# Kernel optimization log

Measured on AMD Instinct MI355X. Metric: run time of the kernel, lower is better.

The kernel has to match this reference:

```python
import jax, jax.numpy as jnp
import numpy as np

C_REG = 50.0  # soft-SVM regularization from __init__ default C=50


def kronecker(A, B):
    # torch: einsum('ab,cd->acbd').view(a*c, b*d)
    return jnp.einsum('ab,cd->acbd', A, B).reshape(
        A.shape[0] * B.shape[0], A.shape[1] * B.shape[1])


def setup_inputs() -> dict:
    key = jax.random.key(0)
    k1, k2, k3, k4 = jax.random.split(key, 4)
    N_c, N_S, N_Q, C, W, H = 16, 25, 15, 3, 32, 32
    D_feat = 640
    S_k = jax.random.normal(k1, (N_c, N_S, C, W, H), dtype=jnp.float32)
    Q_k = jax.random.normal(k2, (N_c, N_Q, C, W, H), dtype=jnp.float32)
    # base_net modeled as Flatten -> Linear(C*W*H, D_feat), no bias
    W_base = jax.random.normal(k3, (C * W * H, D_feat), dtype=jnp.float32) * 0.02
    gamma = jax.random.normal(k4, (1,), dtype=jnp.float32)
    return {"S_k": S_k, "Q_k": Q_k, "W_base": W_base, "gamma": gamma}


def reference(S_k, Q_k, W_base, gamma):
    N_c, N_S = S_k.shape[:2]
    N_Q = Q_k.shape[1]
    # base_net: flatten image dims, project to features
    f_x = S_k.reshape(N_c * N_S, -1) @ W_base  # placeholder
    f_x = Q_k.reshape(N_c * N_Q, -1) @ W_base          # [N_c*N_Q, D]
    K = S_k.reshape(N_c * N_S, -1) @ W_base            # [N_c*N_S, D]
    # kernel matrix + ridge
    aul = K @ K.T + C_REG * jnp.eye(N_c * N_S, dtype=K.dtype)  # [N_c*N_S, N_c*N_S]
    # explicit Kronecker expansion to the full (N_c^2*N_S) system
    Q = kronecker(jnp.eye(N_c, dtype=K.dtype), aul)    # [N_c^2*N_S, N_c^2*N_S]
    p = kronecker(jnp.eye(N_c, dtype=K.dtype),
                  jnp.ones((1, N_S), dtype=K.dtype)).reshape(-1, 1)
    alpha = jnp.linalg.solve(Q, jax.lax.stop_gradient(p))  # p is detached in torch
    alpha = alpha.reshape(N_c, -1)                     # [N_c, N_c*N_S]
    w_k = alpha @ K                                    # [N_c, D]
    logits = -gamma * (f_x @ w_k.T)                    # [N_c*N_Q, N_c]
    return logits
```

## Files before the change

### kernel.cpp

```cpp
#include <hip/hip_runtime.h>
#include <math.h>

#define DIN 3072
#define DF 640
#define MROWS 400
#define QROWS 240
#define NMAT 400
#define PN 416
#define NRHS 16
#define CREG 50.0f
#define PVSTEPS 5
#define CSTEPS 25
#define KSPLIT 4
#define GBLK 13
#define SCOLS 32
#define SPAD 40
#define FPAD 72
#define MTILES 28

typedef __attribute__((ext_vector_type(8))) short bf8v;
typedef __attribute__((ext_vector_type(4))) short s4v;
typedef __attribute__((ext_vector_type(4))) float f32x4;

__device__ __forceinline__ short bf16_rn(float x) {
  unsigned u = __float_as_uint(x);
  u += 0x7FFFu + ((u >> 16) & 1u);
  return (short)(u >> 16);
}
__device__ __forceinline__ void split_sh(float x, short& h, short& l) {
  h = bf16_rn(x);
  float hf = __uint_as_float(((unsigned)(unsigned short)h) << 16);
  l = bf16_rn(x - hf);
}
__device__ __forceinline__ float bf2f(short h) {
  return __uint_as_float(((unsigned)(unsigned short)h) << 16);
}

__global__ __launch_bounds__(256) void gemm_feat_sk(const float* __restrict__ S,
                                                    const float* __restrict__ Qm,
                                                    const float* __restrict__ Wb,
                                                    float* __restrict__ Acc) {
  __shared__ short Ash[64][FPAD];
  __shared__ short Asl[64][FPAD];
  __shared__ short Bsh[64][FPAD];
  __shared__ short Bsl[64][FPAD];
  int tid = threadIdx.x;
  int wave = tid >> 6, lane = tid & 63, l16 = lane & 15, quad = lane >> 4;
  int by = blockIdx.y, bx = blockIdx.x, bz = blockIdx.z;
  int colBase = bx * 64;
  int kbeg = bz * (DIN / KSPLIT), kend = kbeg + (DIN / KSPLIT);
  int arow = by * 64 + (tid >> 4);
  const float* sr = (arow < MROWS) ? (S + (size_t)arow * DIN)
                                   : (Qm + (size_t)(arow - MROWS) * DIN);
  int kc4 = (tid & 15) * 4;
  float4 ar4[4], br4[4];
  auto load_regs = [&](int kk) {
#pragma unroll
    for (int p = 0; p < 4; ++p) {
      int rowoff = 16 * p;
      const float* srp;
      {
        int ar_ = by * 64 + (tid >> 4) + rowoff;
        srp = (ar_ < MROWS) ? (S + (size_t)ar_ * DIN) : (Qm + (size_t)(ar_ - MROWS) * DIN);
      }
      ar4[p] = *reinterpret_cast<const float4*>(srp + kk + kc4);
      int r = (tid >> 4) + rowoff;
      br4[p] = *reinterpret_cast<const float4*>(Wb + (size_t)(kk + r) * DF + colBase + kc4);
    }
  };
  auto split_write = [&]() {
#pragma unroll
    for (int p = 0; p < 4; ++p) {
      int row = (tid >> 4) + 16 * p;
      s4v hv, lv; short h, l;
      split_sh(ar4[p].x, h, l); hv[0] = h; lv[0] = l;
      split_sh(ar4[p].y, h, l); hv[1] = h; lv[1] = l;
      split_sh(ar4[p].z, h, l); hv[2] = h; lv[2] = l;
      split_sh(ar4[p].w, h, l); hv[3] = h; lv[3] = l;
      *reinterpret_cast<s4v*>(&Ash[row][kc4]) = hv;
      *reinterpret_cast<s4v*>(&Asl[row][kc4]) = lv;
      split_sh(br4[p].x, h, l); Bsh[kc4 + 0][row] = h; Bsl[kc4 + 0][row] = l;
      split_sh(br4[p].y, h, l); Bsh[kc4 + 1][row] = h; Bsl[kc4 + 1][row] = l;
      split_sh(br4[p].z, h, l); Bsh[kc4 + 2][row] = h; Bsl[kc4 + 2][row] = l;
      split_sh(br4[p].w, h, l); Bsh[kc4 + 3][row] = h; Bsl[kc4 + 3][row] = l;
    }
  };
  f32x4 acc[4] = {{0,0,0,0},{0,0,0,0},{0,0,0,0},{0,0,0,0}};
  load_regs(kbeg);
  split_write();
  __syncthreads();
  int k0 = kbeg;
  while (true) {
    int kn = k0 + 64;
    bool more = (kn < kend);
    if (more) load_regs(kn);
#pragma unroll
    for (int kk = 0; kk < 64; kk += 32) {
      int ko = kk + quad * 8;
      bf8v ah = *reinterpret_cast<const bf8v*>(&Ash[wave * 16 + l16][ko]);
      bf8v al = *reinterpret_cast<const bf8v*>(&Asl[wave * 16 + l16][ko]);
#pragma unroll
      for (int t = 0; t < 4; ++t) {
        bf8v bh = *reinterpret_cast<const bf8v*>(&Bsh[t * 16 + l16][ko]);
        bf8v bl = *reinterpret_cast<const bf8v*>(&Bsl[t * 16 + l16][ko]);
        acc[t] = __builtin_amdgcn_mfma_f32_16x16x32_bf16(ah, bh, acc[t], 0, 0, 0);
        acc[t] = __builtin_amdgcn_mfma_f32_16x16x32_bf16(ah, bl, acc[t], 0, 0, 0);
        acc[t] = __builtin_amdgcn_mfma_f32_16x16x32_bf16(al, bh, acc[t], 0, 0, 0);
      }
    }
    if (!more) break;
    __syncthreads();
    split_write();
    __syncthreads();
    k0 = kn;
  }
  float* Ap = Acc + (size_t)bz * 640 * DF;
  int row0 = by * 64 + wave * 16;
#pragma unroll
  for (int t = 0; t < 4; ++t)
#pragma unroll
    for (int r = 0; r < 4; ++r) {
      int row = row0 + quad * 4 + r;
      int col = colBase + t * 16 + l16;
      Ap[(size_t)row * DF + col] = acc[t][r];
    }
}

__global__ __launch_bounds__(256) void feat_reduce(const float* __restrict__ Acc,
                                                   short* __restrict__ Kh,
                                                   short* __restrict__ Kl,
                                                   float* __restrict__ FX,
                                                   float* __restrict__ zbuf,
                                                   float* __restrict__ out) {
  int tid = threadIdx.x;
  if (blockIdx.x == 0) {
    for (int e = tid; e < 14160; e += 256) zbuf[e] = 0.f;
  } else if (blockIdx.x == 1) {
    for (int e = tid; e < QROWS * NRHS; e += 256) out[e] = 0.f;
  }
  int idx = blockIdx.x * 256 + tid;
  if (idx >= 640 * DF) return;
  float v = Acc[idx] + Acc[idx + 409600] + Acc[idx + 819200] + Acc[idx + 1228800];
  int row = idx / DF, col = idx - row * DF;
  if (row < MROWS) {
    short h, l; split_sh(v, h, l);
    Kh[(size_t)row * DF + col] = h;
    Kl[(size_t)row * DF + col] = l;
  } else {
    FX[(size_t)(row - MROWS) * DF + col] = v;
  }
}

__global__ __launch_bounds__(256) void gemm_aul(const short* __restrict__ Kh,
                                                const short* __restrict__ Kl,
                                                short* __restrict__ Aph,
                                                short* __restrict__ Apl) {
  int tid = threadIdx.x;
  int wave = tid >> 6, lane = tid & 63;
  int l16 = lane & 15, quad = lane >> 4;
  int row0 = blockIdx.y * 64 + wave * 16;
  int colBase = blockIdx.x * 64;
  bool aValid = (row0 < MROWS);
  const bf8v bzero = {0,0,0,0,0,0,0,0};
  f32x4 acc[4] = {{0,0,0,0},{0,0,0,0},{0,0,0,0},{0,0,0,0}};
  for (int k0 = 0; k0 < DF; k0 += 32) {
    int ka = k0 + quad * 8;
    bf8v ah = bzero, al = bzero;
    if (aValid) {
      size_t ao = (size_t)(row0 + l16) * DF + ka;
      ah = *reinterpret_cast<const bf8v*>(Kh + ao);
      al = *reinterpret_cast<const bf8v*>(Kl + ao);
    }
#pragma unroll
    for (int t = 0; t < 4; ++t) {
      int colt = colBase + t * 16;
      bf8v bh = bzero, bl = bzero;
      if (colt < MROWS) {
        size_t bo = (size_t)(colt + l16) * DF + ka;
        bh = *reinterpret_cast<const bf8v*>(Kh + bo);
        bl = *reinterpret_cast<const bf8v*>(Kl + bo);
      }
      acc[t] = __builtin_amdgcn_mfma_f32_16x16x32_bf16(ah, bh, acc[t], 0, 0, 0);
      acc[t] = __builtin_amdgcn_mfma_f32_16x16x32_bf16(ah, bl, acc[t], 0, 0, 0);
      acc[t] = __builtin_amdgcn_mfma_f32_16x16x32_bf16(al, bh, acc[t], 0, 0, 0);
    }
  }
  if (row0 >= PN) return;
#pragma unroll
  for (int t = 0; t < 4; ++t) {
    int colt = colBase + t * 16;
    if (colt >= PN) continue;
#pragma unroll
    for (int r = 0; r < 4; ++r) {
      int row = row0 + quad * 4 + r;
      int col = colt + l16;
      float v = acc[t][r];
      if (row == col && row < MROWS) v += CREG;
      short h, l; split_sh(v, h, l);
      size_t o = (size_t)row * PN + col;
      Aph[o] = h; Apl[o] = l;
    }
  }
}

__global__ __launch_bounds__(256) void solve_and_m(const short* __restrict__ Aph,
                                                   const short* __restrict__ Apl,
                                                   const float* __restrict__ FX,
                                                   const short* __restrict__ Kh,
                                                   const short* __restrict__ Kl,
                                                   const float* __restrict__ gamma,
                                                   float* __restrict__ Y0,
                                                   float* __restrict__ Y1,
                                                   float* __restrict__ V0,
                                                   float* __restrict__ V1,
                                                   float* __restrict__ rq,
                                                   unsigned* __restrict__ bar,
                                                   unsigned* __restrict__ mflag,
                                                   float* __restrict__ M,
                                                   float* __restrict__ out) {
  int tid = threadIdx.x, b = blockIdx.x;
  int wave = tid >> 6, lane = tid & 63, l16 = lane & 15, quad = lane >> 4;
  const bf8v bzero = {0,0,0,0,0,0,0,0};

  if (b >= GBLK) {
    int mt = b - GBLK;
    int mb = mt / 7, nb = mt - (mt / 7) * 7;
    int q0 = mb * 64 + wave * 16;
    f32x4 acc[4] = {{0,0,0,0},{0,0,0,0},{0,0,0,0},{0,0,0,0}};
    int arow = q0 + l16;
    bool aOk = (arow < QROWS);
    const float* fr = FX + (size_t)(aOk ? arow : 0) * DF;
    for (int k0 = 0; k0 < DF; k0 += 32) {
      int ka = k0 + quad * 8;
      bf8v ah = bzero, al = bzero;
      if (aOk) {
        float4 a0 = *reinterpret_cast<const float4*>(fr + ka);
        float4 a1 = *reinterpret_cast<const float4*>(fr + ka + 4);
        float av[8] = {a0.x, a0.y, a0.z, a0.w, a1.x, a1.y, a1.z, a1.w};
#pragma unroll
        for (int j = 0; j < 8; ++j) { short h, l; split_sh(av[j], h, l); ah[j] = h; al[j] = l; }
      }
#pragma unroll
      for (int t = 0; t < 4; ++t) {
        int n = nb * 64 + t * 16 + l16;
        bf8v bh = bzero, bl = bzero;
        if (n < NMAT) {
          bh = *reinterpret_cast<const bf8v*>(Kh + (size_t)n * DF + ka);
          bl = *reinterpret_cast<const bf8v*>(Kl + (size_t)n * DF + ka);
        }
        acc[t] = __builtin_amdgcn_mfma_f32_16x16x32_bf16(ah, bh, acc[t], 0, 0, 0);
        acc[t] = __builtin_amdgcn_mfma_f32_16x16x32_bf16(ah, bl, acc[t], 0, 0, 0);
        acc[t] = __builtin_amdgcn_mfma_f32_16x16x32_bf16(al, bh, acc[t], 0, 0, 0);
      }
    }
#pragma unroll
    for (int t = 0; t < 4; ++t)
#pragma unroll
      for (int r = 0; r < 4; ++r) {
        int row = q0 + quad * 4 + r;
        int col = nb * 64 + t * 16 + l16;
        if (row < QROWS && col < NMAT)
          __hip_atomic_store(&M[(size_t)row * NMAT + col], acc[t][r],
                             __ATOMIC_RELAXED, __HIP_MEMORY_SCOPE_AGENT);
      }
    __syncthreads();
    if (tid == 0)
      __hip_atomic_fetch_add(mflag, 1u, __ATOMIC_RELEASE, __HIP_MEMORY_SCOPE_AGENT);
    return;
  }

  __shared__ __align__(16) short AsT_h[PN][SPAD];
  __shared__ short AsT_l[PN][SPAD];
  __shared__ short dbT_h[16][SPAD];
  __shared__ short dbT_l[16][SPAD];
  __shared__ float pvp[SCOLS], pvc[SCOLS];
  __shared__ float scal[2];
  __shared__ float XsL[SCOLS][NRHS + 1];
  int r0 = b * SCOLS;

  for (int e = tid; e < SCOLS * (PN / 8); e += 256) {
    int jl = e / (PN / 8), ic = e - (e / (PN / 8)) * (PN / 8);
    bf8v vh = *reinterpret_cast<const bf8v*>(Aph + (size_t)(r0 + jl) * PN + ic * 8);
    bf8v vl = *reinterpret_cast<const bf8v*>(Apl + (size_t)(r0 + jl) * PN + ic * 8);
#pragma unroll
    for (int u = 0; u < 8; ++u) {
      AsT_h[ic * 8 + u][jl] = vh[u];
      AsT_l[ic * 8 + u][jl] = vl[u];
    }
  }
  for (int e = tid; e < 16 * SPAD; e += 256) {
    (&dbT_h[0][0])[e] = 0; (&dbT_l[0][0])[e] = 0;
  }
  __syncthreads();
  if (tid < SCOLS) {
    int gi = r0 + tid;
    float v = (gi < NMAT) ? (1.f + 0.125f * (float)(gi & 7)) : 0.f;
    pvc[tid] = v; pvp[tid] = 0.f;
    dbT_h[0][tid] = bf16_rn(v);
  }
  __syncthreads();

  unsigned ph = 0;
  auto gridbar = [&]() {
    __syncthreads();
    ++ph;
    if (tid == 0) {
      unsigned tgt = ph * GBLK;
      __hip_atomic_fetch_add(bar, 1u, __ATOMIC_RELEASE, __HIP_MEMORY_SCOPE_AGENT);
      while (__hip_atomic_load(bar, __ATOMIC_RELAXED, __HIP_MEMORY_SCOPE_AGENT) < tgt)
        __builtin_amdgcn_s_sleep(2);
    }
    __syncthreads();
  };

  for (int s = 0; s < PVSTEPS; ++s) {
    float* Yv = (s & 1) ? V1 : V0;
    for (int t = wave; t < 26; t += 4) {
      f32x4 acc = {0, 0, 0, 0};
      bf8v bh = *reinterpret_cast<const bf8v*>(&dbT_h[l16][quad * 8]);
      bf8v ah = *reinterpret_cast<const bf8v*>(&AsT_h[t * 16 + l16][quad * 8]);
      acc = __builtin_amdgcn_mfma_f32_16x16x32_bf16(ah, bh, acc, 0, 0, 0);
      if (l16 == 0) {
#pragma unroll
        for (int r_ = 0; r_ < 4; ++r_)
          atomicAdd(&Yv[t * 16 + quad * 4 + r_], acc[r_]);
      }
    }
    gridbar();
    if (tid < SCOLS) {
      float y = atomicExch(&Yv[r0 + tid], 0.f);
      float v = y * (1.f / 4096.f);
      pvp[tid] = pvc[tid];
      pvc[tid] = v;
      dbT_h[0][tid] = bf16_rn(v);
    }
    __syncthreads();
  }
  if (tid == 0) {
    float n = 0.f, dd = 0.f;
    for (int u = 0; u < SCOLS; ++u) { n += pvp[u] * pvc[u]; dd += pvp[u] * pvp[u]; }
    atomicAdd(&rq[0], n);
    atomicAdd(&rq[1], dd);
  }
  gridbar();
  if (tid == 0) {
    float rn = atomicAdd(&rq[0], 0.f), rd = atomicAdd(&rq[1], 0.f);
    float rqv = 4096.f * rn / rd;
    float bb = 1.3f * rqv;
    if (!(bb > 800.f)) bb = 12000.f;
    if (bb > 100000.f) bb = 100000.f;
    scal[0] = 0.5f * (bb + CREG);
    scal[1] = 0.5f * (bb - CREG);
  }
  __syncthreads();
  float theta = scal[0], delta = scal[1];
  float sigma = theta / delta, rho = 1.f / sigma;

  float xr[2], rr[2], dr[2];
#pragma unroll
  for (int m = 0; m < 2; ++m) {
    int rl = (tid >> 4) + 16 * m, c = tid & 15, gi = r0 + rl;
    float pc = (gi < NMAT && (gi / 25) == c) ? 1.f : 0.f;
    xr[m] = 0.f; rr[m] = pc; dr[m] = pc / theta;
    short h, l; split_sh(dr[m], h, l);
    dbT_h[c][rl] = h; dbT_l[c][rl] = l;
  }
  __syncthreads();

  for (int k = 0; k < CSTEPS - 1; ++k) {
    float* Yv = (k & 1) ? Y1 : Y0;
    for (int t = wave; t < 26; t += 4) {
      f32x4 acc = {0, 0, 0, 0};
      bf8v bh = *reinterpret_cast<const bf8v*>(&dbT_h[l16][quad * 8]);
      bf8v bl = *reinterpret_cast<const bf8v*>(&dbT_l[l16][quad * 8]);
      bf8v ah = *reinterpret_cast<const bf8v*>(&AsT_h[t * 16 + l16][quad * 8]);
      bf8v al = *reinterpret_cast<const bf8v*>(&AsT_l[t * 16 + l16][quad * 8]);
      acc = __builtin_amdgcn_mfma_f32_16x16x32_bf16(ah, bh, acc, 0, 0, 0);
      acc = __builtin_amdgcn_mfma_f32_16x16x32_bf16(ah, bl, acc, 0, 0, 0);
      acc = __builtin_amdgcn_mfma_f32_16x16x32_bf16(al, bh, acc, 0, 0, 0);
#pragma unroll
      for (int r_ = 0; r_ < 4; ++r_)
        atomicAdd(&Yv[(t * 16 + quad * 4 + r_) * 16 + l16], acc[r_]);
    }
    gridbar();
    float rho1 = 1.f / (2.f * sigma - rho);
    float s1 = rho1 * rho, s2 = 2.f * rho1 / delta;
    rho = rho1;
#pragma unroll
    for (int m = 0; m < 2; ++m) {
      int rl = (tid >> 4) + 16 * m, c = tid & 15, gi = r0 + rl;
      float mv = atomicExch(&Yv[gi * 16 + c], 0.f);
      xr[m] += dr[m];
      rr[m] -= mv;
      float dn = s1 * dr[m] + s2 * rr[m];
      dr[m] = dn;
      short h, l; split_sh(dn, h, l);
      dbT_h[c][rl] = h; dbT_l[c][rl] = l;
    }
    __syncthreads();
  }
#pragma unroll
  for (int m = 0; m < 2; ++m) {
    int rl = (tid >> 4) + 16 * m, c = tid & 15;
    XsL[rl][c] = xr[m] + dr[m];
  }
  __syncthreads();
  if (tid == 0) {
    while (__hip_atomic_load(mflag, __ATOMIC_RELAXED, __HIP_MEMORY_SCOPE_AGENT) < MTILES)
      __builtin_amdgcn_s_sleep(2);
  }
  __syncthreads();
  float* Msl = reinterpret_cast<float*>(&AsT_h[0][0]);
  for (int e = tid; e < QROWS * SCOLS; e += 256) {
    int q = e >> 5, i = e & 31;
    float v = 0.f;
    if (r0 + i < NMAT)
      v = __hip_atomic_load(&M[(size_t)q * NMAT + r0 + i],
                            __ATOMIC_RELAXED, __HIP_MEMORY_SCOPE_AGENT);
    Msl[e] = v;
  }
  __syncthreads();
  float g = -gamma[0];
  int c = tid & 15;
  for (int q = tid >> 4; q < QROWS; q += 16) {
    float s = 0.f;
#pragma unroll
    for (int i = 0; i < SCOLS; ++i) s += Msl[q * SCOLS + i] * XsL[i][c];
    atomicAdd(&out[q * NRHS + c], g * s);
  }
}

extern "C" void kernel_launch(void* const* d_in, const int* in_sizes, int n_in,
                              void* d_out, int out_size, void* d_ws, size_t ws_size,
                              hipStream_t stream) {
  const float* S = (const float*)d_in[0];
  const float* Qm = (const float*)d_in[1];
  const float* Wb = (const float*)d_in[2];
  const float* gamma = (const float*)d_in[3];
  float* out = (float*)d_out;
  char* base = (char*)d_ws;
  short* Kh   = (short*)(base);
  short* Kl   = (short*)(base + 512000);
  float* FX   = (float*)(base + 1024000);
  short* Aph  = (short*)(base + 1638400);
  short* Apl  = (short*)(base + 1984512);
  float* Mm   = (float*)(base + 2330624);
  unsigned* bar = (unsigned*)(base + 2740224);
  float* rq   = (float*)(base + 2740232);
  unsigned* mflag = (unsigned*)(base + 2740240);
  float* zbuf = (float*)(base + 2740224);
  float* Y0   = (float*)(base + 2740288);
  float* Y1   = (float*)(base + 2766912);
  float* V0   = (float*)(base + 2793536);
  float* V1   = (float*)(base + 2795200);
  float* Acc  = (float*)(base + 2796864);

  gemm_feat_sk<<<dim3(10, 10, KSPLIT), 256, 0, stream>>>(S, Qm, Wb, Acc);
  feat_reduce<<<1600, 256, 0, stream>>>(Acc, Kh, Kl, FX, zbuf, out);
  gemm_aul<<<dim3(7, 7), 256, 0, stream>>>(Kh, Kl, Aph, Apl);
  solve_and_m<<<GBLK + MTILES, 256, 0, stream>>>(Aph, Apl, FX, Kh, Kl, gamma,
                                                 Y0, Y1, V0, V1, rq, bar, mflag,
                                                 Mm, out);
}
```

Before: 229.1 us.

## Switch solver to row-block ownership with broadcast direction vectors instead of atomic partial sums

The Chebyshev/power-iteration solver is restructured. Each block now holds its 32 rows of the matrix untransposed and computes its own slice of the matvec locally, reducing across waves in shared memory. Before, each block computed column contributions and scattered them with global atomicAdd/atomicExch. The direction vector is now packed as hi/lo bf16 in one word, published to global memory, and gathered by every block after a grid barrier. This removes global float atomics and the separate Rayleigh-quotient grid barrier, since every block now computes that quotient redundantly. In exchange, each block does more global reads per step, and the zeroing of the workspace is shrunk.

```diff
diff --git a/kernel.cpp b/kernel.cpp
--- a/kernel.cpp
+++ b/kernel.cpp
@@ -14,9 +14,9 @@
 #define KSPLIT 4
 #define GBLK 13
 #define SCOLS 32
-#define SPAD 40
 #define FPAD 72
 #define MTILES 28
+#define DPAD 424
 
 typedef __attribute__((ext_vector_type(8))) short bf8v;
 typedef __attribute__((ext_vector_type(4))) short s4v;
@@ -49,9 +49,6 @@
   int by = blockIdx.y, bx = blockIdx.x, bz = blockIdx.z;
   int colBase = bx * 64;
   int kbeg = bz * (DIN / KSPLIT), kend = kbeg + (DIN / KSPLIT);
-  int arow = by * 64 + (tid >> 4);
-  const float* sr = (arow < MROWS) ? (S + (size_t)arow * DIN)
-                                   : (Qm + (size_t)(arow - MROWS) * DIN);
   int kc4 = (tid & 15) * 4;
   float4 ar4[4], br4[4];
   auto load_regs = [&](int kk) {
@@ -134,7 +131,7 @@
                                                    float* __restrict__ out) {
   int tid = threadIdx.x;
   if (blockIdx.x == 0) {
-    for (int e = tid; e < 14160; e += 256) zbuf[e] = 0.f;
+    for (int e = tid; e < 16; e += 256) zbuf[e] = 0.f;
   } else if (blockIdx.x == 1) {
     for (int e = tid; e < QROWS * NRHS; e += 256) out[e] = 0.f;
   }
@@ -209,11 +206,10 @@
                                                    const short* __restrict__ Kh,
                                                    const short* __restrict__ Kl,
                                                    const float* __restrict__ gamma,
-                                                   float* __restrict__ Y0,
-                                                   float* __restrict__ Y1,
+                                                   unsigned* __restrict__ D0,
+                                                   unsigned* __restrict__ D1,
                                                    float* __restrict__ V0,
                                                    float* __restrict__ V1,
-                                                   float* __restrict__ rq,
                                                    unsigned* __restrict__ bar,
                                                    unsigned* __restrict__ mflag,
                                                    float* __restrict__ M,
@@ -269,34 +265,27 @@
     return;
   }
 
-  __shared__ __align__(16) short AsT_h[PN][SPAD];
-  __shared__ short AsT_l[PN][SPAD];
-  __shared__ short dbT_h[16][SPAD];
-  __shared__ short dbT_l[16][SPAD];
-  __shared__ float pvp[SCOLS], pvc[SCOLS];
+  __shared__ __align__(16) short Abig[2][SCOLS][DPAD];
+  __shared__ __align__(16) short dbT[2][NRHS][DPAD];
+  __shared__ float yred[4][SCOLS][17];
+  __shared__ float vprevL[PN], vcurL[PN];
+  __shared__ float XsL[SCOLS][NRHS + 1];
   __shared__ float scal[2];
-  __shared__ float XsL[SCOLS][NRHS + 1];
+  __shared__ float rn[4], rd[4];
   int r0 = b * SCOLS;
 
-  for (int e = tid; e < SCOLS * (PN / 8); e += 256) {
-    int jl = e / (PN / 8), ic = e - (e / (PN / 8)) * (PN / 8);
-    bf8v vh = *reinterpret_cast<const bf8v*>(Aph + (size_t)(r0 + jl) * PN + ic * 8);
-    bf8v vl = *reinterpret_cast<const bf8v*>(Apl + (size_t)(r0 + jl) * PN + ic * 8);
-#pragma unroll
-    for (int u = 0; u < 8; ++u) {
-      AsT_h[ic * 8 + u][jl] = vh[u];
-      AsT_l[ic * 8 + u][jl] = vl[u];
-    }
-  }
-  for (int e = tid; e < 16 * SPAD; e += 256) {
-    (&dbT_h[0][0])[e] = 0; (&dbT_l[0][0])[e] = 0;
-  }
-  __syncthreads();
-  if (tid < SCOLS) {
-    int gi = r0 + tid;
-    float v = (gi < NMAT) ? (1.f + 0.125f * (float)(gi & 7)) : 0.f;
-    pvc[tid] = v; pvp[tid] = 0.f;
-    dbT_h[0][tid] = bf16_rn(v);
+  for (int e = tid; e < SCOLS * 52; e += 256) {
+    int i = e / 52, c = e - i * 52;
+    *reinterpret_cast<bf8v*>(&Abig[0][i][c * 8]) =
+        *reinterpret_cast<const bf8v*>(Aph + (size_t)(r0 + i) * PN + c * 8);
+    *reinterpret_cast<bf8v*>(&Abig[1][i][c * 8]) =
+        *reinterpret_cast<const bf8v*>(Apl + (size_t)(r0 + i) * PN + c * 8);
+  }
+  for (int e = tid; e < NRHS * DPAD; e += 256) (&dbT[0][0][0])[e] = 0;
+  for (int e = tid; e < PN; e += 256) {
+    float v = (e < NMAT) ? (1.f + 0.125f * (float)(e & 7)) : 0.f;
+    vcurL[e] = v;
+    dbT[0][0][e] = bf16_rn(v);
   }
   __syncthreads();
 
@@ -313,46 +302,86 @@
     __syncthreads();
   };
 
+  auto matvec = [&](bool lo) {
+    f32x4 acc0 = {0, 0, 0, 0}, acc1 = {0, 0, 0, 0};
+    for (int kt = wave; kt < 13; kt += 4) {
+      int ko = kt * 32 + quad * 8;
+      bf8v bh = *reinterpret_cast<const bf8v*>(&dbT[0][l16][ko]);
+      bf8v ah0 = *reinterpret_cast<const bf8v*>(&Abig[0][l16][ko]);
+      bf8v ah1 = *reinterpret_cast<const bf8v*>(&Abig[0][16 + l16][ko]);
+      acc0 = __builtin_amdgcn_mfma_f32_16x16x32_bf16(ah0, bh, acc0, 0, 0, 0);
+      acc1 = __builtin_amdgcn_mfma_f32_16x16x32_bf16(ah1, bh, acc1, 0, 0, 0);
+      if (lo) {
+        bf8v bl = *reinterpret_cast<const bf8v*>(&dbT[1][l16][ko]);
+        bf8v al0 = *reinterpret_cast<const bf8v*>(&Abig[1][l16][ko]);
+        bf8v al1 = *reinterpret_cast<const bf8v*>(&Abig[1][16 + l16][ko]);
+        acc0 = __builtin_amdgcn_mfma_f32_16x16x32_bf16(ah0, bl, acc0, 0, 0, 0);
+        acc0 = __builtin_amdgcn_mfma_f32_16x16x32_bf16(al0, bh, acc0, 0, 0, 0);
+        acc1 = __builtin_amdgcn_mfma_f32_16x16x32_bf16(ah1, bl, acc1, 0, 0, 0);
+        acc1 = __builtin_amdgcn_mfma_f32_16x16x32_bf16(al1, bh, acc1, 0, 0, 0);
+      }
+    }
+#pragma unroll
+    for (int r_ = 0; r_ < 4; ++r_) {
+      yred[wave][quad * 4 + r_][l16] = acc0[r_];
+      yred[wave][16 + quad * 4 + r_][l16] = acc1[r_];
+    }
+  };
+
   for (int s = 0; s < PVSTEPS; ++s) {
-    float* Yv = (s & 1) ? V1 : V0;
-    for (int t = wave; t < 26; t += 4) {
-      f32x4 acc = {0, 0, 0, 0};
-      bf8v bh = *reinterpret_cast<const bf8v*>(&dbT_h[l16][quad * 8]);
-      bf8v ah = *reinterpret_cast<const bf8v*>(&AsT_h[t * 16 + l16][quad * 8]);
-      acc = __builtin_amdgcn_mfma_f32_16x16x32_bf16(ah, bh, acc, 0, 0, 0);
-      if (l16 == 0) {
-#pragma unroll
-        for (int r_ = 0; r_ < 4; ++r_)
-          atomicAdd(&Yv[t * 16 + quad * 4 + r_], acc[r_]);
-      }
+    matvec(false);
+    __syncthreads();
+    if (tid < SCOLS) {
+      float y = yred[0][tid][0] + yred[1][tid][0] + yred[2][tid][0] + yred[3][tid][0];
+      float* Vb = (s & 1) ? V1 : V0;
+      __hip_atomic_store(&Vb[r0 + tid], y, __ATOMIC_RELAXED, __HIP_MEMORY_SCOPE_AGENT);
     }
     gridbar();
-    if (tid < SCOLS) {
-      float y = atomicExch(&Yv[r0 + tid], 0.f);
-      float v = y * (1.f / 4096.f);
-      pvp[tid] = pvc[tid];
-      pvc[tid] = v;
-      dbT_h[0][tid] = bf16_rn(v);
-    }
-    __syncthreads();
-  }
-  if (tid == 0) {
+    const float* Vb = (s & 1) ? V1 : V0;
+    if (s == PVSTEPS - 1)
+      for (int e = tid; e < PN; e += 256) vprevL[e] = vcurL[e];
+    float g0 = __hip_atomic_load(&Vb[tid], __ATOMIC_RELAXED, __HIP_MEMORY_SCOPE_AGENT);
+    float g1 = (tid < PN - 256)
+        ? __hip_atomic_load(&Vb[tid + 256], __ATOMIC_RELAXED, __HIP_MEMORY_SCOPE_AGENT)
+        : 0.f;
+    {
+      float v = g0 * (1.f / 4096.f);
+      vcurL[tid] = v;
+      dbT[0][0][tid] = bf16_rn(v);
+    }
+    if (tid < PN - 256) {
+      float v = g1 * (1.f / 4096.f);
+      vcurL[tid + 256] = v;
+      dbT[0][0][tid + 256] = bf16_rn(v);
+    }
+    __syncthreads();
+  }
+
+  {
     float n = 0.f, dd = 0.f;
-    for (int u = 0; u < SCOLS; ++u) { n += pvp[u] * pvc[u]; dd += pvp[u] * pvp[u]; }
-    atomicAdd(&rq[0], n);
-    atomicAdd(&rq[1], dd);
-  }
-  gridbar();
-  if (tid == 0) {
-    float rn = atomicAdd(&rq[0], 0.f), rd = atomicAdd(&rq[1], 0.f);
-    float rqv = 4096.f * rn / rd;
-    float bb = 1.3f * rqv;
-    if (!(bb > 800.f)) bb = 12000.f;
-    if (bb > 100000.f) bb = 100000.f;
-    scal[0] = 0.5f * (bb + CREG);
-    scal[1] = 0.5f * (bb - CREG);
-  }
-  __syncthreads();
+    for (int e = tid; e < PN; e += 256) {
+      n += vprevL[e] * vcurL[e];
+      dd += vprevL[e] * vprevL[e];
+    }
+#pragma unroll
+    for (int o = 32; o; o >>= 1) {
+      n += __shfl_down(n, o);
+      dd += __shfl_down(dd, o);
+    }
+    if (lane == 0) { rn[wave] = n; rd[wave] = dd; }
+    __syncthreads();
+    if (tid == 0) {
+      float N = rn[0] + rn[1] + rn[2] + rn[3];
+      float D = rd[0] + rd[1] + rd[2] + rd[3];
+      float rqv = 4096.f * N / D;
+      float bb = 1.3f * rqv;
+      if (!(bb > 800.f)) bb = 12000.f;
+      if (bb > 100000.f) bb = 100000.f;
+      scal[0] = 0.5f * (bb + CREG);
+      scal[1] = 0.5f * (bb - CREG);
+    }
+    __syncthreads();
+  }
   float theta = scal[0], delta = scal[1];
   float sigma = theta / delta, rho = 1.f / sigma;
 
@@ -363,42 +392,63 @@
     float pc = (gi < NMAT && (gi / 25) == c) ? 1.f : 0.f;
     xr[m] = 0.f; rr[m] = pc; dr[m] = pc / theta;
     short h, l; split_sh(dr[m], h, l);
-    dbT_h[c][rl] = h; dbT_l[c][rl] = l;
+    __hip_atomic_store(&D0[(size_t)gi * NRHS + c],
+                       ((unsigned)(unsigned short)h << 16) | (unsigned)(unsigned short)l,
+                       __ATOMIC_RELAXED, __HIP_MEMORY_SCOPE_AGENT);
+  }
+  gridbar();
+  {
+    unsigned gw[26];
+#pragma unroll
+    for (int j = 0; j < 26; ++j)
+      gw[j] = __hip_atomic_load(&D0[tid + 256 * j], __ATOMIC_RELAXED, __HIP_MEMORY_SCOPE_AGENT);
+#pragma unroll
+    for (int j = 0; j < 26; ++j) {
+      int e = tid + 256 * j, row = e >> 4, c = e & 15;
+      dbT[0][c][row] = (short)(gw[j] >> 16);
+      dbT[1][c][row] = (short)gw[j];
+    }
   }
   __syncthreads();
 
   for (int k = 0; k < CSTEPS - 1; ++k) {
-    float* Yv = (k & 1) ? Y1 : Y0;
-    for (int t = wave; t < 26; t += 4) {
-      f32x4 acc = {0, 0, 0, 0};
-      bf8v bh = *reinterpret_cast<const bf8v*>(&dbT_h[l16][quad * 8]);
-      bf8v bl = *reinterpret_cast<const bf8v*>(&dbT_l[l16][quad * 8]);
-      bf8v ah = *reinterpret_cast<const bf8v*>(&AsT_h[t * 16 + l16][quad * 8]);
-      bf8v al = *reinterpret_cast<const bf8v*>(&AsT_l[t * 16 + l16][quad * 8]);
-      acc = __builtin_amdgcn_mfma_f32_16x16x32_bf16(ah, bh, acc, 0, 0, 0);
-      acc = __builtin_amdgcn_mfma_f32_16x16x32_bf16(ah, bl, acc, 0, 0, 0);
-      acc = __builtin_amdgcn_mfma_f32_16x16x32_bf16(al, bh, acc, 0, 0, 0);
-#pragma unroll
-      for (int r_ = 0; r_ < 4; ++r_)
-        atomicAdd(&Yv[(t * 16 + quad * 4 + r_) * 16 + l16], acc[r_]);
-    }
-    gridbar();
+    matvec(true);
+    __syncthreads();
     float rho1 = 1.f / (2.f * sigma - rho);
     float s1 = rho1 * rho, s2 = 2.f * rho1 / delta;
     rho = rho1;
+    unsigned* Db = (k & 1) ? D0 : D1;
 #pragma unroll
     for (int m = 0; m < 2; ++m) {
       int rl = (tid >> 4) + 16 * m, c = tid & 15, gi = r0 + rl;
-      float mv = atomicExch(&Yv[gi * 16 + c], 0.f);
+      float mv = yred[0][rl][c] + yred[1][rl][c] + yred[2][rl][c] + yred[3][rl][c];
       xr[m] += dr[m];
       rr[m] -= mv;
       float dn = s1 * dr[m] + s2 * rr[m];
       dr[m] = dn;
-      short h, l; split_sh(dn, h, l);
-      dbT_h[c][rl] = h; dbT_l[c][rl] = l;
-    }
-    __syncthreads();
-  }
+      if (k < CSTEPS - 2) {
+        short h, l; split_sh(dn, h, l);
+        __hip_atomic_store(&Db[(size_t)gi * NRHS + c],
+                           ((unsigned)(unsigned short)h << 16) | (unsigned)(unsigned short)l,
+                           __ATOMIC_RELAXED, __HIP_MEMORY_SCOPE_AGENT);
+      }
+    }
+    if (k < CSTEPS - 2) {
+      gridbar();
+      unsigned gw[26];
+#pragma unroll
+      for (int j = 0; j < 26; ++j)
+        gw[j] = __hip_atomic_load(&Db[tid + 256 * j], __ATOMIC_RELAXED, __HIP_MEMORY_SCOPE_AGENT);
+#pragma unroll
+      for (int j = 0; j < 26; ++j) {
+        int e = tid + 256 * j, row = e >> 4, c = e & 15;
+        dbT[0][c][row] = (short)(gw[j] >> 16);
+        dbT[1][c][row] = (short)gw[j];
+      }
+    }
+    __syncthreads();
+  }
+
 #pragma unroll
   for (int m = 0; m < 2; ++m) {
     int rl = (tid >> 4) + 16 * m, c = tid & 15;
@@ -410,14 +460,20 @@
       __builtin_amdgcn_s_sleep(2);
   }
   __syncthreads();
-  float* Msl = reinterpret_cast<float*>(&AsT_h[0][0]);
-  for (int e = tid; e < QROWS * SCOLS; e += 256) {
-    int q = e >> 5, i = e & 31;
-    float v = 0.f;
-    if (r0 + i < NMAT)
-      v = __hip_atomic_load(&M[(size_t)q * NMAT + r0 + i],
-                            __ATOMIC_RELAXED, __HIP_MEMORY_SCOPE_AGENT);
-    Msl[e] = v;
+  float* Msl = reinterpret_cast<float*>(&Abig[0][0][0]);
+  {
+    float gm[30];
+#pragma unroll
+    for (int j = 0; j < 30; ++j) {
+      int e = tid + 256 * j;
+      int q = e >> 5, i = e & 31;
+      gm[j] = (r0 + i < NMAT)
+                  ? __hip_atomic_load(&M[(size_t)q * NMAT + r0 + i],
+                                      __ATOMIC_RELAXED, __HIP_MEMORY_SCOPE_AGENT)
+                  : 0.f;
+    }
+#pragma unroll
+    for (int j = 0; j < 30; ++j) Msl[tid + 256 * j] = gm[j];
   }
   __syncthreads();
   float g = -gamma[0];
@@ -446,11 +502,10 @@
   short* Apl  = (short*)(base + 1984512);
   float* Mm   = (float*)(base + 2330624);
   unsigned* bar = (unsigned*)(base + 2740224);
-  float* rq   = (float*)(base + 2740232);
   unsigned* mflag = (unsigned*)(base + 2740240);
   float* zbuf = (float*)(base + 2740224);
-  float* Y0   = (float*)(base + 2740288);
-  float* Y1   = (float*)(base + 2766912);
+  unsigned* D0 = (unsigned*)(base + 2740288);
+  unsigned* D1 = (unsigned*)(base + 2766912);
   float* V0   = (float*)(base + 2793536);
   float* V1   = (float*)(base + 2795200);
   float* Acc  = (float*)(base + 2796864);
@@ -459,6 +514,6 @@
   feat_reduce<<<1600, 256, 0, stream>>>(Acc, Kh, Kl, FX, zbuf, out);
   gemm_aul<<<dim3(7, 7), 256, 0, stream>>>(Kh, Kl, Aph, Apl);
   solve_and_m<<<GBLK + MTILES, 256, 0, stream>>>(Aph, Apl, FX, Kh, Kl, gamma,
-                                                 Y0, Y1, V0, V1, rq, bar, mflag,
+                                                 D0, D1, V0, V1, bar, mflag,
                                                  Mm, out);
 }
```

Result: faster. 216.0 us (-5.7%).

## Solve each right-hand side in its own block, dropping grid barriers

Applied to the files above, without the earlier changes.

The Chebyshev solve moves from 13 blocks, each owning a row slice and synchronising through global atomics and grid barriers, to 16 independent blocks, each owning one right-hand side. Each block runs the whole matvec by streaming A from global memory (L2). This removes the grid-wide spin barriers and the atomic accumulation traffic on every iteration. The cost is that every block repeats the power iteration and rereads the full matrix each step, and the MFMA uses only one useful column out of 16. The feature GEMM split-K also doubles from 4 to 8, which doubles the partial-sum traffic in the reduce kernel.

```diff
diff --git a/kernel.cpp b/kernel.cpp
--- a/kernel.cpp
+++ b/kernel.cpp
@@ -11,10 +11,8 @@
 #define CREG 50.0f
 #define PVSTEPS 5
 #define CSTEPS 25
-#define KSPLIT 4
-#define GBLK 13
-#define SCOLS 32
-#define SPAD 40
+#define KSPLIT 8
+#define SRHS 16
 #define FPAD 72
 #define MTILES 28
 
@@ -31,9 +29,6 @@
   h = bf16_rn(x);
   float hf = __uint_as_float(((unsigned)(unsigned short)h) << 16);
   l = bf16_rn(x - hf);
-}
-__device__ __forceinline__ float bf2f(short h) {
-  return __uint_as_float(((unsigned)(unsigned short)h) << 16);
 }
 
 __global__ __launch_bounds__(256) void gemm_feat_sk(const float* __restrict__ S,
@@ -49,9 +44,6 @@
   int by = blockIdx.y, bx = blockIdx.x, bz = blockIdx.z;
   int colBase = bx * 64;
   int kbeg = bz * (DIN / KSPLIT), kend = kbeg + (DIN / KSPLIT);
-  int arow = by * 64 + (tid >> 4);
-  const float* sr = (arow < MROWS) ? (S + (size_t)arow * DIN)
-                                   : (Qm + (size_t)(arow - MROWS) * DIN);
   int kc4 = (tid & 15) * 4;
   float4 ar4[4], br4[4];
   auto load_regs = [&](int kk) {
@@ -130,17 +122,16 @@
                                                    short* __restrict__ Kh,
                                                    short* __restrict__ Kl,
                                                    float* __restrict__ FX,
-                                                   float* __restrict__ zbuf,
-                                                   float* __restrict__ out) {
+                                                   float* __restrict__ zbuf) {
   int tid = threadIdx.x;
   if (blockIdx.x == 0) {
-    for (int e = tid; e < 14160; e += 256) zbuf[e] = 0.f;
-  } else if (blockIdx.x == 1) {
-    for (int e = tid; e < QROWS * NRHS; e += 256) out[e] = 0.f;
+    if (tid < 16) zbuf[tid] = 0.f;
   }
   int idx = blockIdx.x * 256 + tid;
   if (idx >= 640 * DF) return;
-  float v = Acc[idx] + Acc[idx + 409600] + Acc[idx + 819200] + Acc[idx + 1228800];
+  float v = 0.f;
+#pragma unroll
+  for (int s = 0; s < KSPLIT; ++s) v += Acc[idx + (size_t)s * 409600];
   int row = idx / DF, col = idx - row * DF;
   if (row < MROWS) {
     short h, l; split_sh(v, h, l);
@@ -209,12 +200,6 @@
                                                    const short* __restrict__ Kh,
                                                    const short* __restrict__ Kl,
                                                    const float* __restrict__ gamma,
-                                                   float* __restrict__ Y0,
-                                                   float* __restrict__ Y1,
-                                                   float* __restrict__ V0,
-                                                   float* __restrict__ V1,
-                                                   float* __restrict__ rq,
-                                                   unsigned* __restrict__ bar,
                                                    unsigned* __restrict__ mflag,
                                                    float* __restrict__ M,
                                                    float* __restrict__ out) {
@@ -222,8 +207,8 @@
   int wave = tid >> 6, lane = tid & 63, l16 = lane & 15, quad = lane >> 4;
   const bf8v bzero = {0,0,0,0,0,0,0,0};
 
-  if (b >= GBLK) {
-    int mt = b - GBLK;
+  if (b >= SRHS) {
+    int mt = b - SRHS;
     int mb = mt / 7, nb = mt - (mt / 7) * 7;
     int q0 = mb * 64 + wave * 16;
     f32x4 acc[4] = {{0,0,0,0},{0,0,0,0},{0,0,0,0},{0,0,0,0}};
@@ -269,164 +254,136 @@
     return;
   }
 
-  __shared__ __align__(16) short AsT_h[PN][SPAD];
-  __shared__ short AsT_l[PN][SPAD];
-  __shared__ short dbT_h[16][SPAD];
-  __shared__ short dbT_l[16][SPAD];
-  __shared__ float pvp[SCOLS], pvc[SCOLS];
+  int c = b;
+  __shared__ __align__(16) short dbh[432], dbl[432];
+  __shared__ float ys[PN];
+  __shared__ float xf[PN], rf[PN], df[PN];
+  __shared__ float vprev[PN], vcur[PN];
   __shared__ float scal[2];
-  __shared__ float XsL[SCOLS][NRHS + 1];
-  int r0 = b * SCOLS;
-
-  for (int e = tid; e < SCOLS * (PN / 8); e += 256) {
-    int jl = e / (PN / 8), ic = e - (e / (PN / 8)) * (PN / 8);
-    bf8v vh = *reinterpret_cast<const bf8v*>(Aph + (size_t)(r0 + jl) * PN + ic * 8);
-    bf8v vl = *reinterpret_cast<const bf8v*>(Apl + (size_t)(r0 + jl) * PN + ic * 8);
-#pragma unroll
-    for (int u = 0; u < 8; ++u) {
-      AsT_h[ic * 8 + u][jl] = vh[u];
-      AsT_l[ic * 8 + u][jl] = vl[u];
-    }
-  }
-  for (int e = tid; e < 16 * SPAD; e += 256) {
-    (&dbT_h[0][0])[e] = 0; (&dbT_l[0][0])[e] = 0;
+  __shared__ float rn4[4], rd4[4];
+
+  auto matvec = [&](bool lo) {
+    for (int rg = wave; rg < 26; rg += 4) {
+      const short* arow_h = Aph + (size_t)(rg * 16 + l16) * PN;
+      const short* arow_l = Apl + (size_t)(rg * 16 + l16) * PN;
+      f32x4 acc = {0, 0, 0, 0};
+#pragma unroll
+      for (int kc = 0; kc < 13; ++kc) {
+        int ko = kc * 32 + quad * 8;
+        bf8v ah = *reinterpret_cast<const bf8v*>(arow_h + ko);
+        bf8v bh = bzero, bl = bzero;
+        if (l16 == 0) {
+          bh = *reinterpret_cast<const bf8v*>(&dbh[ko]);
+          if (lo) bl = *reinterpret_cast<const bf8v*>(&dbl[ko]);
+        }
+        acc = __builtin_amdgcn_mfma_f32_16x16x32_bf16(ah, bh, acc, 0, 0, 0);
+        if (lo) {
+          bf8v al = *reinterpret_cast<const bf8v*>(arow_l + ko);
+          acc = __builtin_amdgcn_mfma_f32_16x16x32_bf16(ah, bl, acc, 0, 0, 0);
+          acc = __builtin_amdgcn_mfma_f32_16x16x32_bf16(al, bh, acc, 0, 0, 0);
+        }
+      }
+      if (l16 == 0) {
+#pragma unroll
+        for (int r = 0; r < 4; ++r) ys[rg * 16 + quad * 4 + r] = acc[r];
+      }
+    }
+  };
+
+  for (int e = tid; e < PN; e += 256) {
+    float v = (e < NMAT) ? (1.f + 0.125f * (float)(e & 7)) : 0.f;
+    vcur[e] = v;
+    dbh[e] = bf16_rn(v);
+    dbl[e] = 0;
   }
   __syncthreads();
-  if (tid < SCOLS) {
-    int gi = r0 + tid;
-    float v = (gi < NMAT) ? (1.f + 0.125f * (float)(gi & 7)) : 0.f;
-    pvc[tid] = v; pvp[tid] = 0.f;
-    dbT_h[0][tid] = bf16_rn(v);
-  }
-  __syncthreads();
-
-  unsigned ph = 0;
-  auto gridbar = [&]() {
-    __syncthreads();
-    ++ph;
+
+  for (int s = 0; s < PVSTEPS; ++s) {
+    matvec(false);
+    __syncthreads();
+    for (int e = tid; e < PN; e += 256) {
+      if (s == PVSTEPS - 1) vprev[e] = vcur[e];
+      float v = ys[e] * (1.f / 4096.f);
+      vcur[e] = v;
+      dbh[e] = bf16_rn(v);
+    }
+    __syncthreads();
+  }
+
+  {
+    float n = 0.f, dd = 0.f;
+    for (int e = tid; e < PN; e += 256) {
+      n += vprev[e] * vcur[e];
+      dd += vprev[e] * vprev[e];
+    }
+#pragma unroll
+    for (int o = 32; o; o >>= 1) {
+      n += __shfl_down(n, o);
+      dd += __shfl_down(dd, o);
+    }
+    if (lane == 0) { rn4[wave] = n; rd4[wave] = dd; }
+    __syncthreads();
     if (tid == 0) {
-      unsigned tgt = ph * GBLK;
-      __hip_atomic_fetch_add(bar, 1u, __ATOMIC_RELEASE, __HIP_MEMORY_SCOPE_AGENT);
-      while (__hip_atomic_load(bar, __ATOMIC_RELAXED, __HIP_MEMORY_SCOPE_AGENT) < tgt)
-        __builtin_amdgcn_s_sleep(2);
-    }
-    __syncthreads();
-  };
-
-  for (int s = 0; s < PVSTEPS; ++s) {
-    float* Yv = (s & 1) ? V1 : V0;
-    for (int t = wave; t < 26; t += 4) {
-      f32x4 acc = {0, 0, 0, 0};
-      bf8v bh = *reinterpret_cast<const bf8v*>(&dbT_h[l16][quad * 8]);
-      bf8v ah = *reinterpret_cast<const bf8v*>(&AsT_h[t * 16 + l16][quad * 8]);
-      acc = __builtin_amdgcn_mfma_f32_16x16x32_bf16(ah, bh, acc, 0, 0, 0);
-      if (l16 == 0) {
-#pragma unroll
-        for (int r_ = 0; r_ < 4; ++r_)
-          atomicAdd(&Yv[t * 16 + quad * 4 + r_], acc[r_]);
-      }
-    }
-    gridbar();
-    if (tid < SCOLS) {
-      float y = atomicExch(&Yv[r0 + tid], 0.f);
-      float v = y * (1.f / 4096.f);
-      pvp[tid] = pvc[tid];
-      pvc[tid] = v;
-      dbT_h[0][tid] = bf16_rn(v);
-    }
-    __syncthreads();
-  }
-  if (tid == 0) {
-    float n = 0.f, dd = 0.f;
-    for (int u = 0; u < SCOLS; ++u) { n += pvp[u] * pvc[u]; dd += pvp[u] * pvp[u]; }
-    atomicAdd(&rq[0], n);
-    atomicAdd(&rq[1], dd);
-  }
-  gridbar();
-  if (tid == 0) {
-    float rn = atomicAdd(&rq[0], 0.f), rd = atomicAdd(&rq[1], 0.f);
-    float rqv = 4096.f * rn / rd;
-    float bb = 1.3f * rqv;
-    if (!(bb > 800.f)) bb = 12000.f;
-    if (bb > 100000.f) bb = 100000.f;
-    scal[0] = 0.5f * (bb + CREG);
-    scal[1] = 0.5f * (bb - CREG);
-  }
-  __syncthreads();
+      float N = rn4[0] + rn4[1] + rn4[2] + rn4[3];
+      float D = rd4[0] + rd4[1] + rd4[2] + rd4[3];
+      float rqv = 4096.f * N / D;
+      float bb = 1.3f * rqv;
+      if (!(bb > 800.f)) bb = 12000.f;
+      if (bb > 100000.f) bb = 100000.f;
+      scal[0] = 0.5f * (bb + CREG);
+      scal[1] = 0.5f * (bb - CREG);
+    }
+    __syncthreads();
+  }
   float theta = scal[0], delta = scal[1];
   float sigma = theta / delta, rho = 1.f / sigma;
 
-  float xr[2], rr[2], dr[2];
-#pragma unroll
-  for (int m = 0; m < 2; ++m) {
-    int rl = (tid >> 4) + 16 * m, c = tid & 15, gi = r0 + rl;
-    float pc = (gi < NMAT && (gi / 25) == c) ? 1.f : 0.f;
-    xr[m] = 0.f; rr[m] = pc; dr[m] = pc / theta;
-    short h, l; split_sh(dr[m], h, l);
-    dbT_h[c][rl] = h; dbT_l[c][rl] = l;
+  for (int e = tid; e < PN; e += 256) {
+    float pc = (e < NMAT && (e / 25) == c) ? 1.f : 0.f;
+    xf[e] = 0.f; rf[e] = pc;
+    float d0 = pc / theta;
+    df[e] = d0;
+    short h, l; split_sh(d0, h, l);
+    dbh[e] = h; dbl[e] = l;
   }
   __syncthreads();
 
   for (int k = 0; k < CSTEPS - 1; ++k) {
-    float* Yv = (k & 1) ? Y1 : Y0;
-    for (int t = wave; t < 26; t += 4) {
-      f32x4 acc = {0, 0, 0, 0};
-      bf8v bh = *reinterpret_cast<const bf8v*>(&dbT_h[l16][quad * 8]);
-      bf8v bl = *reinterpret_cast<const bf8v*>(&dbT_l[l16][quad * 8]);
-      bf8v ah = *reinterpret_cast<const bf8v*>(&AsT_h[t * 16 + l16][quad * 8]);
-      bf8v al = *reinterpret_cast<const bf8v*>(&AsT_l[t * 16 + l16][quad * 8]);
-      acc = __builtin_amdgcn_mfma_f32_16x16x32_bf16(ah, bh, acc, 0, 0, 0);
-      acc = __builtin_amdgcn_mfma_f32_16x16x32_bf16(ah, bl, acc, 0, 0, 0);
-      acc = __builtin_amdgcn_mfma_f32_16x16x32_bf16(al, bh, acc, 0, 0, 0);
-#pragma unroll
-      for (int r_ = 0; r_ < 4; ++r_)
-        atomicAdd(&Yv[(t * 16 + quad * 4 + r_) * 16 + l16], acc[r_]);
-    }
-    gridbar();
+    matvec(true);
+    __syncthreads();
     float rho1 = 1.f / (2.f * sigma - rho);
     float s1 = rho1 * rho, s2 = 2.f * rho1 / delta;
     rho = rho1;
-#pragma unroll
-    for (int m = 0; m < 2; ++m) {
-      int rl = (tid >> 4) + 16 * m, c = tid & 15, gi = r0 + rl;
-      float mv = atomicExch(&Yv[gi * 16 + c], 0.f);
-      xr[m] += dr[m];
-      rr[m] -= mv;
-      float dn = s1 * dr[m] + s2 * rr[m];
-      dr[m] = dn;
+    for (int e = tid; e < PN; e += 256) {
+      float mv = ys[e];
+      xf[e] += df[e];
+      rf[e] -= mv;
+      float dn = s1 * df[e] + s2 * rf[e];
+      df[e] = dn;
       short h, l; split_sh(dn, h, l);
-      dbT_h[c][rl] = h; dbT_l[c][rl] = l;
-    }
-    __syncthreads();
-  }
-#pragma unroll
-  for (int m = 0; m < 2; ++m) {
-    int rl = (tid >> 4) + 16 * m, c = tid & 15;
-    XsL[rl][c] = xr[m] + dr[m];
-  }
+      dbh[e] = h; dbl[e] = l;
+    }
+    __syncthreads();
+  }
+
+  for (int e = tid; e < PN; e += 256) vcur[e] = xf[e] + df[e];
   __syncthreads();
+
   if (tid == 0) {
     while (__hip_atomic_load(mflag, __ATOMIC_RELAXED, __HIP_MEMORY_SCOPE_AGENT) < MTILES)
       __builtin_amdgcn_s_sleep(2);
   }
   __syncthreads();
-  float* Msl = reinterpret_cast<float*>(&AsT_h[0][0]);
-  for (int e = tid; e < QROWS * SCOLS; e += 256) {
-    int q = e >> 5, i = e & 31;
-    float v = 0.f;
-    if (r0 + i < NMAT)
-      v = __hip_atomic_load(&M[(size_t)q * NMAT + r0 + i],
-                            __ATOMIC_RELAXED, __HIP_MEMORY_SCOPE_AGENT);
-    Msl[e] = v;
-  }
-  __syncthreads();
   float g = -gamma[0];
-  int c = tid & 15;
-  for (int q = tid >> 4; q < QROWS; q += 16) {
+  for (int q = tid; q < QROWS; q += 256) {
+    const float* mr = M + (size_t)q * NMAT;
     float s = 0.f;
-#pragma unroll
-    for (int i = 0; i < SCOLS; ++i) s += Msl[q * SCOLS + i] * XsL[i][c];
-    atomicAdd(&out[q * NRHS + c], g * s);
+#pragma unroll 4
+    for (int i = 0; i < NMAT; i += 4) {
+      float4 m4 = *reinterpret_cast<const float4*>(mr + i);
+      s += m4.x * vcur[i] + m4.y * vcur[i + 1] + m4.z * vcur[i + 2] + m4.w * vcur[i + 3];
+    }
+    out[q * NRHS + c] = g * s;
   }
 }
 
@@ -445,20 +402,13 @@
   short* Aph  = (short*)(base + 1638400);
   short* Apl  = (short*)(base + 1984512);
   float* Mm   = (float*)(base + 2330624);
-  unsigned* bar = (unsigned*)(base + 2740224);
-  float* rq   = (float*)(base + 2740232);
   unsigned* mflag = (unsigned*)(base + 2740240);
   float* zbuf = (float*)(base + 2740224);
-  float* Y0   = (float*)(base + 2740288);
-  float* Y1   = (float*)(base + 2766912);
-  float* V0   = (float*)(base + 2793536);
-  float* V1   = (float*)(base + 2795200);
   float* Acc  = (float*)(base + 2796864);
 
   gemm_feat_sk<<<dim3(10, 10, KSPLIT), 256, 0, stream>>>(S, Qm, Wb, Acc);
-  feat_reduce<<<1600, 256, 0, stream>>>(Acc, Kh, Kl, FX, zbuf, out);
+  feat_reduce<<<1600, 256, 0, stream>>>(Acc, Kh, Kl, FX, zbuf);
   gemm_aul<<<dim3(7, 7), 256, 0, stream>>>(Kh, Kl, Aph, Apl);
-  solve_and_m<<<GBLK + MTILES, 256, 0, stream>>>(Aph, Apl, FX, Kh, Kl, gamma,
-                                                 Y0, Y1, V0, V1, rq, bar, mflag,
-                                                 Mm, out);
-}
+  solve_and_m<<<SRHS + MTILES, 256, 0, stream>>>(Aph, Apl, FX, Kh, Kl, gamma,
+                                                 mflag, Mm, out);
+}
```

Result: slower. 505.4 us (+120.6%).
